# Optimization experiments

Hardware: AMD Instinct MI355X
Metric: run time of the kernel (lower is better)

The kernel has to match this reference:

```python
import jax, jax.numpy as jnp
import numpy as np

EPS = 1e-8  # torch nn.CosineSimilarity default eps


def setup_inputs() -> dict:
    key = jax.random.key(0)
    k1, k2 = jax.random.split(key)
    support_set = jax.random.normal(k1, (50000, 512), dtype=jnp.float32)
    query_set = jax.random.normal(k2, (2048, 512), dtype=jnp.float32)
    return {"support_set": support_set, "query_set": query_set}


def reference(support_set, query_set):
    # torch: cos(x1, x2) = x1.x2 / max(||x1|| * ||x2||, eps), per row.
    # Loop over queries fused into one matmul: out[q, n] = cos(support[n], query[q]).
    dots = jnp.einsum("qd,nd->qn", query_set, support_set)        # [Q, N]
    s_norm = jnp.linalg.norm(support_set, axis=1)                  # [N]
    q_norm = jnp.linalg.norm(query_set, axis=1)                    # [Q]
    denom = jnp.maximum(q_norm[:, None] * s_norm[None, :], EPS)    # [Q, N]
    return dots / denom
```

## Files before the change

### kernel.cpp

```cpp
#include <hip/hip_runtime.h>
#include <stdint.h>

#define NSUP   50000
#define NSUPP  50176
#define NQRY   2048
#define KD     512
#define BK     32
#define NKT    16

typedef __attribute__((ext_vector_type(8))) short bf16x8;
typedef __attribute__((ext_vector_type(4))) float f32x4;

__device__ __forceinline__ unsigned short f2bf(float f) {
  unsigned int u = __float_as_uint(f);
  u += 0x7FFFu + ((u >> 16) & 1u);
  return (unsigned short)(u >> 16);
}

__global__ __launch_bounds__(256) void prep_kernel(
    const float* __restrict__ sup, const float* __restrict__ qry,
    unsigned short* __restrict__ s_bf, unsigned short* __restrict__ q_bf) {
  const int row  = blockIdx.x * 4 + (threadIdx.x >> 6);
  const int lane = threadIdx.x & 63;

  const float* src = nullptr;
  unsigned short* dst;
  if (row < NSUPP) {
    dst = s_bf + (size_t)row * KD;
    if (row < NSUP) src = sup + (size_t)row * KD;
  } else {
    const int r = row - NSUPP;
    dst = q_bf + (size_t)r * KD;
    src = qry + (size_t)r * KD;
  }

  if (src == nullptr) {
    bf16x8 z = {};
    *(bf16x8*)(dst + lane * 8) = z;
    return;
  }

  const float4 v0 = ((const float4*)src)[lane * 2 + 0];
  const float4 v1 = ((const float4*)src)[lane * 2 + 1];
  float ss = v0.x*v0.x + v0.y*v0.y + v0.z*v0.z + v0.w*v0.w
           + v1.x*v1.x + v1.y*v1.y + v1.z*v1.z + v1.w*v1.w;
  #pragma unroll
  for (int off = 32; off > 0; off >>= 1) ss += __shfl_xor(ss, off);
  const float inv = rsqrtf(fmaxf(ss, 1e-30f));

  bf16x8 o;
  o[0]=(short)f2bf(v0.x*inv); o[1]=(short)f2bf(v0.y*inv);
  o[2]=(short)f2bf(v0.z*inv); o[3]=(short)f2bf(v0.w*inv);
  o[4]=(short)f2bf(v1.x*inv); o[5]=(short)f2bf(v1.y*inv);
  o[6]=(short)f2bf(v1.z*inv); o[7]=(short)f2bf(v1.w*inv);
  *(bf16x8*)(dst + lane * 8) = o;
}

__device__ __forceinline__ void stage_unit(const unsigned short* __restrict__ g,
                                           unsigned short* lds, int grow_base,
                                           int kt, int w, int l) {
  const int chunk = (l & 3) ^ ((l >> 3) & 3);
  #pragma unroll
  for (int i = 0; i < 2; ++i) {
    const unsigned short* src = g + (size_t)(grow_base + i*64 + w*16 + (l>>2)) * KD
                                  + kt*BK + chunk*8;
    unsigned short* dst = lds + i*2048 + w*512;
    __builtin_amdgcn_global_load_lds(
        (const __attribute__((address_space(1))) void*)src,
        (__attribute__((address_space(3))) void*)dst, 16, 0, 0);
  }
}

#define SWZ_OFF(R, hi) (((hi) ^ (((R) >> 1) & 3)) * 8)

__global__ __launch_bounds__(256, 3) void gemm_kernel(
    const unsigned short* __restrict__ S,
    const unsigned short* __restrict__ Q,
    float* __restrict__ out) {
  __shared__ __attribute__((aligned(16))) unsigned short As[2][128][BK];
  __shared__ __attribute__((aligned(16))) unsigned short Bs[2][128][BK];

  const int tid = threadIdx.x;
  const int w = tid >> 6, l = tid & 63;
  const int wr = w >> 1, wc = w & 1;
  const int rof = l & 15, hi = l >> 4;

  const int orig  = blockIdx.x;
  const int xcd   = orig & 7;
  const int idx   = orig >> 3;
  const int stile = xcd * 49 + (idx >> 4);
  const int qtile = idx & 15;
  const int ts = stile * 128;
  const int tq = qtile * 128;

  f32x4 acc[4][4] = {};

  stage_unit(S, &As[0][0][0], ts, 0, w, l);
  stage_unit(Q, &Bs[0][0][0], tq, 0, w, l);
  __syncthreads();

  #pragma unroll
  for (int t = 0; t < NKT; ++t) {
    const int slot = t & 1;
    if (t + 1 < NKT) {
      stage_unit(S, &As[slot ^ 1][0][0], ts, t + 1, w, l);
      stage_unit(Q, &Bs[slot ^ 1][0][0], tq, t + 1, w, l);
    }

    bf16x8 a[4], b[4];
    #pragma unroll
    for (int i = 0; i < 4; ++i) {
      const int R = wr*64 + i*16 + rof;
      a[i] = *(const bf16x8*)&As[slot][R][SWZ_OFF(R, hi)];
    }
    #pragma unroll
    for (int i = 0; i < 4; ++i) {
      const int R = wc*64 + i*16 + rof;
      b[i] = *(const bf16x8*)&Bs[slot][R][SWZ_OFF(R, hi)];
    }

    #pragma unroll
    for (int mi = 0; mi < 4; ++mi)
      #pragma unroll
      for (int ni = 0; ni < 4; ++ni)
        acc[mi][ni] = __builtin_amdgcn_mfma_f32_16x16x32_bf16(a[mi], b[ni], acc[mi][ni], 0, 0, 0);

    __syncthreads();
  }

  #pragma unroll
  for (int mi = 0; mi < 4; ++mi) {
    const int s = ts + wr*64 + mi*16 + hi*4;
    if (s < NSUP) {
      #pragma unroll
      for (int ni = 0; ni < 4; ++ni) {
        const int q = tq + wc*64 + ni*16 + rof;
        __builtin_nontemporal_store(acc[mi][ni],
                                    (f32x4*)(out + (size_t)q * NSUP + s));
      }
    }
  }
}

extern "C" void kernel_launch(void* const* d_in, const int* in_sizes, int n_in,
                              void* d_out, int out_size, void* d_ws, size_t ws_size,
                              hipStream_t stream) {
  const float* sup = (const float*)d_in[0];
  const float* qry = (const float*)d_in[1];
  float* out = (float*)d_out;

  char* ws = (char*)d_ws;
  unsigned short* s_bf = (unsigned short*)(ws);
  unsigned short* q_bf = (unsigned short*)(ws + (size_t)NSUPP * KD * 2);

  prep_kernel<<<(NSUPP + NQRY) / 4, 256, 0, stream>>>(sup, qry, s_bf, q_bf);

  gemm_kernel<<<6272, 256, 0, stream>>>(s_bf, q_bf, out);
}
```

Before: 202.2 us.

## Keep full support tile resident in LDS and stream pre-swizzled query fragments

Each block now loads one 128-row support tile with the full K=512 depth into 128KB of dynamic LDS once, then loops over all 16 query tiles. The per-K-step double-buffered staging and its barriers go away. The prep kernel writes the normalized queries in an MFMA-fragment-ready layout, so waves load B operands straight from global/L2 with one coalesced 16-byte load per lane. The grid shrinks to 392 blocks of 512 threads with one block per CU. That risks wave-quantization imbalance across CUs, more L2 traffic for query fragments, and no overlap between global loads and MFMA.

```diff
diff --git a/kernel.cpp b/kernel.cpp
--- a/kernel.cpp
+++ b/kernel.cpp
@@ -5,8 +5,8 @@
 #define NSUPP  50176
 #define NQRY   2048
 #define KD     512
-#define BK     32
 #define NKT    16
+#define NQT    16
 
 typedef __attribute__((ext_vector_type(8))) short bf16x8;
 typedef __attribute__((ext_vector_type(4))) float f32x4;
@@ -19,24 +19,24 @@
 
 __global__ __launch_bounds__(256) void prep_kernel(
     const float* __restrict__ sup, const float* __restrict__ qry,
-    unsigned short* __restrict__ s_bf, unsigned short* __restrict__ q_bf) {
+    unsigned short* __restrict__ s_bf, unsigned short* __restrict__ Qf) {
   const int row  = blockIdx.x * 4 + (threadIdx.x >> 6);
   const int lane = threadIdx.x & 63;
 
   const float* src = nullptr;
-  unsigned short* dst;
+  bool is_q = false;
+  int q = 0;
   if (row < NSUPP) {
-    dst = s_bf + (size_t)row * KD;
     if (row < NSUP) src = sup + (size_t)row * KD;
   } else {
-    const int r = row - NSUPP;
-    dst = q_bf + (size_t)r * KD;
-    src = qry + (size_t)r * KD;
+    q = row - NSUPP;
+    src = qry + (size_t)q * KD;
+    is_q = true;
   }
 
   if (src == nullptr) {
     bf16x8 z = {};
-    *(bf16x8*)(dst + lane * 8) = z;
+    *(bf16x8*)(s_bf + (size_t)row * KD + lane * 8) = z;
     return;
   }
 
@@ -53,90 +53,76 @@
   o[2]=(short)f2bf(v0.z*inv); o[3]=(short)f2bf(v0.w*inv);
   o[4]=(short)f2bf(v1.x*inv); o[5]=(short)f2bf(v1.y*inv);
   o[6]=(short)f2bf(v1.z*inv); o[7]=(short)f2bf(v1.w*inv);
-  *(bf16x8*)(dst + lane * 8) = o;
+
+  if (!is_q) {
+    *(bf16x8*)(s_bf + (size_t)row * KD + lane * 8) = o;
+  } else {
+    const int q16 = q >> 4, rq = q & 15;
+    const int kt = lane >> 2, hi = lane & 3;
+    const int ldst = hi * 16 + rq;
+    *(bf16x8*)(Qf + ((size_t)(q16 * 16 + kt) * 64 + ldst) * 8) = o;
+  }
 }
 
-__device__ __forceinline__ void stage_unit(const unsigned short* __restrict__ g,
-                                           unsigned short* lds, int grow_base,
-                                           int kt, int w, int l) {
-  const int chunk = (l & 3) ^ ((l >> 3) & 3);
+__global__ __launch_bounds__(512, 1) void gemm_kernel(
+    const unsigned short* __restrict__ S,
+    const unsigned short* __restrict__ Qf,
+    float* __restrict__ out) {
+  extern __shared__ unsigned short Sl[];
+
+  const int tid = threadIdx.x;
+  const int w = tid >> 6, l = tid & 63;
+  const int wr = w >> 2, wn = w & 3;
+  const int rof = l & 15, hi = l >> 4;
+  const int ts = blockIdx.x * 128;
+
   #pragma unroll
-  for (int i = 0; i < 2; ++i) {
-    const unsigned short* src = g + (size_t)(grow_base + i*64 + w*16 + (l>>2)) * KD
-                                  + kt*BK + chunk*8;
-    unsigned short* dst = lds + i*2048 + w*512;
+  for (int i = 0; i < 16; ++i) {
+    const int row = i * 8 + w;
+    const unsigned short* src = S + (size_t)(ts + row) * KD + ((l ^ w) * 8);
+    unsigned short* dst = Sl + row * KD + l * 8;
     __builtin_amdgcn_global_load_lds(
         (const __attribute__((address_space(1))) void*)src,
         (__attribute__((address_space(3))) void*)dst, 16, 0, 0);
   }
-}
-
-#define SWZ_OFF(R, hi) (((hi) ^ (((R) >> 1) & 3)) * 8)
-
-__global__ __launch_bounds__(256, 3) void gemm_kernel(
-    const unsigned short* __restrict__ S,
-    const unsigned short* __restrict__ Q,
-    float* __restrict__ out) {
-  __shared__ __attribute__((aligned(16))) unsigned short As[2][128][BK];
-  __shared__ __attribute__((aligned(16))) unsigned short Bs[2][128][BK];
-
-  const int tid = threadIdx.x;
-  const int w = tid >> 6, l = tid & 63;
-  const int wr = w >> 1, wc = w & 1;
-  const int rof = l & 15, hi = l >> 4;
-
-  const int orig  = blockIdx.x;
-  const int xcd   = orig & 7;
-  const int idx   = orig >> 3;
-  const int stile = xcd * 49 + (idx >> 4);
-  const int qtile = idx & 15;
-  const int ts = stile * 128;
-  const int tq = qtile * 128;
-
-  f32x4 acc[4][4] = {};
-
-  stage_unit(S, &As[0][0][0], ts, 0, w, l);
-  stage_unit(Q, &Bs[0][0][0], tq, 0, w, l);
   __syncthreads();
 
-  #pragma unroll
-  for (int t = 0; t < NKT; ++t) {
-    const int slot = t & 1;
-    if (t + 1 < NKT) {
-      stage_unit(S, &As[slot ^ 1][0][0], ts, t + 1, w, l);
-      stage_unit(Q, &Bs[slot ^ 1][0][0], tq, t + 1, w, l);
-    }
+  #pragma unroll 1
+  for (int qt = 0; qt < NQT; ++qt) {
+    f32x4 acc[4][2] = {};
 
-    bf16x8 a[4], b[4];
     #pragma unroll
-    for (int i = 0; i < 4; ++i) {
-      const int R = wr*64 + i*16 + rof;
-      a[i] = *(const bf16x8*)&As[slot][R][SWZ_OFF(R, hi)];
-    }
-    #pragma unroll
-    for (int i = 0; i < 4; ++i) {
-      const int R = wc*64 + i*16 + rof;
-      b[i] = *(const bf16x8*)&Bs[slot][R][SWZ_OFF(R, hi)];
+    for (int kt = 0; kt < NKT; ++kt) {
+      bf16x8 b[2];
+      #pragma unroll
+      for (int i = 0; i < 2; ++i) {
+        const int q16 = qt * 8 + wn * 2 + i;
+        b[i] = *(const bf16x8*)(Qf + ((size_t)(q16 * 16 + kt) * 64 + l) * 8);
+      }
+      bf16x8 a[4];
+      #pragma unroll
+      for (int i = 0; i < 4; ++i) {
+        const int R = wr * 64 + i * 16 + rof;
+        const int g = (kt * 4 + hi) ^ (R & 7);
+        a[i] = *(const bf16x8*)(Sl + R * KD + g * 8);
+      }
+      #pragma unroll
+      for (int mi = 0; mi < 4; ++mi)
+        #pragma unroll
+        for (int ni = 0; ni < 2; ++ni)
+          acc[mi][ni] = __builtin_amdgcn_mfma_f32_16x16x32_bf16(a[mi], b[ni], acc[mi][ni], 0, 0, 0);
     }
 
     #pragma unroll
-    for (int mi = 0; mi < 4; ++mi)
-      #pragma unroll
-      for (int ni = 0; ni < 4; ++ni)
-        acc[mi][ni] = __builtin_amdgcn_mfma_f32_16x16x32_bf16(a[mi], b[ni], acc[mi][ni], 0, 0, 0);
-
-    __syncthreads();
-  }
-
-  #pragma unroll
-  for (int mi = 0; mi < 4; ++mi) {
-    const int s = ts + wr*64 + mi*16 + hi*4;
-    if (s < NSUP) {
-      #pragma unroll
-      for (int ni = 0; ni < 4; ++ni) {
-        const int q = tq + wc*64 + ni*16 + rof;
-        __builtin_nontemporal_store(acc[mi][ni],
-                                    (f32x4*)(out + (size_t)q * NSUP + s));
+    for (int mi = 0; mi < 4; ++mi) {
+      const int s = ts + wr * 64 + mi * 16 + hi * 4;
+      if (s < NSUP) {
+        #pragma unroll
+        for (int ni = 0; ni < 2; ++ni) {
+          const int q = qt * 128 + wn * 32 + ni * 16 + rof;
+          __builtin_nontemporal_store(acc[mi][ni],
+                                      (f32x4*)(out + (size_t)q * NSUP + s));
+        }
       }
     }
   }
@@ -151,9 +137,9 @@
 
   char* ws = (char*)d_ws;
   unsigned short* s_bf = (unsigned short*)(ws);
-  unsigned short* q_bf = (unsigned short*)(ws + (size_t)NSUPP * KD * 2);
+  unsigned short* Qf   = (unsigned short*)(ws + (size_t)NSUPP * KD * 2);
 
-  prep_kernel<<<(NSUPP + NQRY) / 4, 256, 0, stream>>>(sup, qry, s_bf, q_bf);
+  prep_kernel<<<(NSUPP + NQRY) / 4, 256, 0, stream>>>(sup, qry, s_bf, Qf);
 
-  gemm_kernel<<<6272, 256, 0, stream>>>(s_bf, q_bf, out);
+  gemm_kernel<<<392, 512, 131072, stream>>>(s_bf, Qf, out);
 }
```

After: 674.2 us. 233% more time.
